# Performance work log

Hardware: AMD Instinct MI355X
Metric: run time of the kernel (lower is better)

The kernel has to match this reference:

```python
import jax, jax.numpy as jnp
import numpy as np

HEADS = 8
HC = 64  # num_head_channels
DIM = 256
HIDDEN = HEADS * HC
EPS = 1e-5


def setup_inputs() -> dict:
    key = jax.random.key(0)
    ks = jax.random.split(key, 6)
    x = jax.random.normal(ks[0], (16, DIM, 64, 64), dtype=jnp.float32)
    Wq = jax.random.normal(ks[1], (HIDDEN, DIM), dtype=jnp.float32) * 0.02
    Wk = jax.random.normal(ks[2], (HIDDEN, DIM), dtype=jnp.float32) * 0.02
    Wv = jax.random.normal(ks[3], (HIDDEN, DIM), dtype=jnp.float32) * 0.02
    Wo = jax.random.normal(ks[4], (DIM, HIDDEN), dtype=jnp.float32) * 0.02
    bo = jnp.zeros((DIM,), dtype=jnp.float32)
    gamma = jnp.ones((DIM,), dtype=jnp.float32)
    beta = jnp.zeros((DIM,), dtype=jnp.float32)
    return {"x": x, "Wq": Wq, "Wk": Wk, "Wv": Wv, "Wo": Wo, "bo": bo,
            "gamma": gamma, "beta": beta}


def reference(x, Wq, Wk, Wv, Wo, bo, gamma, beta):
    b, c, h, w = x.shape
    n = h * w
    scale = HC ** (-0.5)
    xf = x.reshape(b, c, n)  # [b, c, n]
    # 1x1 convs == channel matmuls
    q = jnp.einsum('oc,bcn->bon', Wq, xf).reshape(b * HEADS, HC, n)
    k = jnp.einsum('oc,bcn->bon', Wk, xf).reshape(b * HEADS, HC, n)
    v = jnp.einsum('oc,bcn->bon', Wv, xf).reshape(b * HEADS, HC, n)
    q = jax.nn.softmax(q, axis=1) * scale      # softmax over head channels
    k = jax.nn.softmax(k, axis=2)              # softmax over spatial
    # context = k @ v^T : [bh, hc, hc]
    context = jnp.einsum('bdn,ben->bde', k, v)
    # output = context^T @ q : [bh, hc, n]
    out = jnp.einsum('bde,bdn->ben', context, q)
    out = out.reshape(b, HIDDEN, n)
    # to_out conv1x1 + bias
    y = jnp.einsum('oc,bcn->bon', Wo, out) + bo[None, :, None]
    # GroupNorm(num_groups=1): normalize over (c, n) per sample
    mean = jnp.mean(y, axis=(1, 2), keepdims=True)
    var = jnp.var(y, axis=(1, 2), keepdims=True)
    y = (y - mean) * jax.lax.rsqrt(var + EPS)
    y = y * gamma[None, :, None] + beta[None, :, None]
    return y.reshape(b, c, h, w) + x
```

## Files before the change

### kernel.cpp

```cpp
#include <hip/hip_runtime.h>
#include <hip/hip_bf16.h>

#define DEV __device__ __forceinline__

constexpr int B_ = 16, CDIM = 256, NDIM = 4096, HID = 512, HEADS = 8, HC = 64;
constexpr float EPSV = 1e-5f;

using bf16x8 = __attribute__((ext_vector_type(8))) __bf16;
using f32x4  = __attribute__((ext_vector_type(4))) float;
using s16x8  = __attribute__((ext_vector_type(8))) short;
using s16x4  = __attribute__((ext_vector_type(4))) short;

DEV short f2bf(float f) {
  __hip_bfloat16 h = __float2bfloat16(f);
  return *reinterpret_cast<short*>(&h);
}
DEV f32x4 MFMA(bf16x8 a, bf16x8 b, f32x4 c) {
  return __builtin_amdgcn_mfma_f32_16x16x32_bf16(a, b, c, 0, 0, 0);
}

__global__ void wconv_kernel(const float* __restrict__ Wq, const float* __restrict__ Wk,
                             const float* __restrict__ Wv, const float* __restrict__ Wo,
                             short* __restrict__ Wall, short* __restrict__ Wo_b) {
  const int i = blockIdx.x * 256 + threadIdx.x;
  const int nw = HID * CDIM;
  if (i < nw) Wall[i] = f2bf(Wq[i]);
  else if (i < 2 * nw) Wall[i] = f2bf(Wk[i - nw]);
  else if (i < 3 * nw) Wall[i] = f2bf(Wv[i - 2 * nw]);
  if (i < CDIM * HID) Wo_b[i] = f2bf(Wo[i]);
}

__global__ __launch_bounds__(256) void xconv_kernel(const float* __restrict__ x, short* __restrict__ xt) {
  __shared__ float t[32][33];
  const int bi = blockIdx.z, n0 = blockIdx.x * 32, c0 = blockIdx.y * 32;
  const int tx = threadIdx.x, ty = threadIdx.y;
  const float* xb = x + (size_t)bi * CDIM * NDIM;
#pragma unroll
  for (int i = 0; i < 32; i += 8)
    t[ty + i][tx] = xb[(size_t)(c0 + ty + i) * NDIM + n0 + tx];
  __syncthreads();
  short* xtb = xt + (size_t)bi * NDIM * CDIM;
#pragma unroll
  for (int i = 0; i < 32; i += 8)
    xtb[(size_t)(n0 + ty + i) * CDIM + c0 + tx] = f2bf(t[tx][ty + i]);
}

DEV bf16x8 xs_read(const char* xs, int row, int colShorts) {
  int byte = (row << 9) + (colShorts << 1);
  byte ^= (row & 7) << 4;
  return *(const bf16x8*)(xs + byte);
}

__global__ __launch_bounds__(256) void kvslice_kernel(const short* __restrict__ Wall,
                                                      const short* __restrict__ xt,
                                                      float* __restrict__ ctxp,
                                                      float* __restrict__ statp,
                                                      int nper) {
  const int bh = blockIdx.x, sl = blockIdx.y, nsl = gridDim.y;
  const int bi = bh >> 3, h = bh & 7;
  const int tid = threadIdx.x, lane = tid & 63, wid = tid >> 6;
  const int ro = lane & 15, g = lane >> 4, ko = g * 8;
  const short* Wk = Wall + (size_t)(HID + h * HC) * CDIM;
  const short* Wv = Wall + (size_t)(2 * HID + h * HC) * CDIM;
  const char* xbase = (const char*)(xt + ((size_t)bi * NDIM + (size_t)sl * nper) * CDIM);

  __shared__ __align__(16) char xs[64 * 512];
  __shared__ short pl[64][68];
  __shared__ short vl[64][68];

  bf16x8 ak[8], av[8];
#pragma unroll
  for (int ks = 0; ks < 8; ++ks) {
    ak[ks] = *(const bf16x8*)&Wk[(size_t)(wid * 16 + ro) * CDIM + ks * 32 + ko];
    av[ks] = *(const bf16x8*)&Wv[(size_t)(wid * 16 + ro) * CDIM + ks * 32 + ko];
  }
  float sacc[4] = {0.f, 0.f, 0.f, 0.f};
  f32x4 cacc[4] = {};
  const int drow = wid * 16 + g * 4;

  s16x8 r[8];
#pragma unroll
  for (int it = 0; it < 8; ++it) r[it] = *(const s16x8*)(xbase + it * 4096 + tid * 16);

  for (int nc = 0; nc < nper; nc += 64) {
    if (nc > 0) {
#pragma unroll
      for (int ks = 0; ks < 2; ++ks) {
        bf16x8 pa = *(const bf16x8*)&pl[wid * 16 + ro][ks * 32 + ko];
#pragma unroll
        for (int et = 0; et < 4; ++et) {
          bf16x8 vb = *(const bf16x8*)&vl[et * 16 + ro][ks * 32 + ko];
          cacc[et] = MFMA(pa, vb, cacc[et]);
        }
      }
    }
#pragma unroll
    for (int it = 0; it < 8; ++it) {
      const int fb = it * 4096 + tid * 16;
      *(s16x8*)(xs + (fb ^ (((fb >> 9) & 7) << 4))) = r[it];
    }
    __syncthreads();
    if (nc + 64 < nper) {
      const char* srcn = xbase + (size_t)(nc + 64) * 512;
#pragma unroll
      for (int it = 0; it < 8; ++it) r[it] = *(const s16x8*)(srcn + it * 4096 + tid * 16);
    }
    f32x4 kacc[4] = {};
    f32x4 vacc[4] = {};
#pragma unroll
    for (int ks = 0; ks < 8; ++ks)
#pragma unroll
      for (int nt = 0; nt < 4; ++nt) {
        bf16x8 bfr = xs_read(xs, nt * 16 + ro, ks * 32 + ko);
        kacc[nt] = MFMA(ak[ks], bfr, kacc[nt]);
        vacc[nt] = MFMA(av[ks], bfr, vacc[nt]);
      }
#pragma unroll
    for (int nt = 0; nt < 4; ++nt)
#pragma unroll
      for (int j = 0; j < 4; ++j) {
        const float p = __expf(kacc[nt][j]);
        sacc[j] += p;
        pl[drow + j][nt * 16 + ro] = f2bf(p);
        vl[drow + j][nt * 16 + ro] = f2bf(vacc[nt][j]);
      }
    __syncthreads();
  }
#pragma unroll
  for (int ks = 0; ks < 2; ++ks) {
    bf16x8 pa = *(const bf16x8*)&pl[wid * 16 + ro][ks * 32 + ko];
#pragma unroll
    for (int et = 0; et < 4; ++et) {
      bf16x8 vb = *(const bf16x8*)&vl[et * 16 + ro][ks * 32 + ko];
      cacc[et] = MFMA(pa, vb, cacc[et]);
    }
  }
#pragma unroll
  for (int o = 1; o < 16; o <<= 1)
#pragma unroll
    for (int j = 0; j < 4; ++j) sacc[j] += __shfl_xor(sacc[j], o);

  float* cp = ctxp + ((size_t)bh * nsl + sl) * HC * HC;
#pragma unroll
  for (int et = 0; et < 4; ++et)
#pragma unroll
    for (int j = 0; j < 4; ++j)
      cp[(drow + j) * HC + et * 16 + ro] = cacc[et][j];
  if (ro == 0) {
    float* sp = statp + ((size_t)bh * nsl + sl) * HC;
#pragma unroll
    for (int j = 0; j < 4; ++j) sp[drow + j] = sacc[j];
  }
}

__global__ __launch_bounds__(256) void ctxred_kernel(const float* __restrict__ ctxp,
                                                     const float* __restrict__ statp,
                                                     short* __restrict__ ctx, int nsl) {
  const int bh = blockIdx.x, tid = threadIdx.x;
  const int d = tid >> 2, e0 = (tid & 3) * 16;
  const float* sp = statp + (size_t)bh * nsl * HC;
  float stot = 0.f;
  for (int i = 0; i < nsl; ++i) stot += sp[i * HC + d];
  const float inv = 1.f / stot;
  const float* cp = ctxp + (size_t)bh * nsl * HC * HC;
  short* cb = ctx + (size_t)bh * HC * HC;
  for (int e = e0; e < e0 + 16; ++e) {
    float u = 0.f;
    for (int i = 0; i < nsl; ++i) u += cp[i * HC * HC + d * HC + e];
    cb[d * HC + e] = f2bf(u * inv);
  }
}

__global__ __launch_bounds__(256) void meff_kernel(const short* __restrict__ Wo_b,
                                                   const short* __restrict__ ctx,
                                                   short* __restrict__ Meff) {
  const int bh = blockIdx.x, bi = bh >> 3, h = bh & 7;
  const int tid = threadIdx.x, lane = tid & 63, wid = tid >> 6;
  const int ro = lane & 15, ko = (lane >> 4) * 8;
  const short* Arow = Wo_b + h * HC;
  const short* Bc = ctx + (size_t)bh * HC * HC;
  f32x4 acc[4][4] = {};
#pragma unroll
  for (int ks = 0; ks < 64; ks += 32) {
    bf16x8 af[4], bv[4];
#pragma unroll
    for (int mi = 0; mi < 4; ++mi)
      af[mi] = *(const bf16x8*)&Arow[(size_t)(wid * 64 + mi * 16 + ro) * HID + ks + ko];
#pragma unroll
    for (int ni = 0; ni < 4; ++ni)
      bv[ni] = *(const bf16x8*)&Bc[(ni * 16 + ro) * HC + ks + ko];
#pragma unroll
    for (int mi = 0; mi < 4; ++mi)
#pragma unroll
      for (int ni = 0; ni < 4; ++ni) acc[mi][ni] = MFMA(af[mi], bv[ni], acc[mi][ni]);
  }
  short* Mb = Meff + (size_t)bi * CDIM * HID + h * HC;
  const int r0 = wid * 64 + ((lane >> 4) << 2), c0 = lane & 15;
#pragma unroll
  for (int mi = 0; mi < 4; ++mi)
#pragma unroll
    for (int ni = 0; ni < 4; ++ni)
#pragma unroll
      for (int j = 0; j < 4; ++j)
        Mb[(size_t)(r0 + mi * 16 + j) * HID + ni * 16 + c0] = f2bf(acc[mi][ni][j]);
}

__global__ __launch_bounds__(256) void qsm_kernel(const short* __restrict__ Wall,
                                                  const short* __restrict__ xt,
                                                  short* __restrict__ qtc,
                                                  int NC, int nbase) {
  const int bi = blockIdx.y, n0 = blockIdx.x * 64;
  const int tid = threadIdx.x, lane = tid & 63, wid = tid >> 6;
  const int ro = lane & 15, g = lane >> 4, ko = g * 8;
  __shared__ __align__(16) char xs[64 * 512];
  __shared__ float ps[8 * 4 * 4 * 16];
  const char* xbase = (const char*)(xt + ((size_t)bi * NDIM + nbase + n0) * CDIM);
#pragma unroll
  for (int it = 0; it < 8; ++it) {
    const int fb = it * 4096 + tid * 16;
    *(s16x8*)(xs + (fb ^ (((fb >> 9) & 7) << 4))) = *(const s16x8*)(xbase + fb);
  }
  __syncthreads();

  const short* wbase = Wall + (size_t)(wid * 16 + ro) * CDIM + ko;
  bf16x8 aq[8], aqn[8];
#pragma unroll
  for (int ks = 0; ks < 8; ++ks) aq[ks] = *(const bf16x8*)(wbase + ks * 32);

#pragma unroll 1
  for (int h = 0; h < HEADS; ++h) {
    if (h < 7) {
      const short* wn = wbase + (size_t)(h + 1) * HC * CDIM;
#pragma unroll
      for (int ks = 0; ks < 8; ++ks) aqn[ks] = *(const bf16x8*)(wn + ks * 32);
    }
    f32x4 kacc[4] = {};
#pragma unroll
    for (int ks = 0; ks < 8; ++ks)
#pragma unroll
      for (int nt = 0; nt < 4; ++nt)
        kacc[nt] = MFMA(aq[ks], xs_read(xs, nt * 16 + ro, ks * 32 + ko), kacc[nt]);
    float tsum[4];
#pragma unroll
    for (int nt = 0; nt < 4; ++nt) {
#pragma unroll
      for (int j = 0; j < 4; ++j) kacc[nt][j] = __expf(kacc[nt][j]);
      tsum[nt] = kacc[nt][0] + kacc[nt][1] + kacc[nt][2] + kacc[nt][3];
    }
#pragma unroll
    for (int nt = 0; nt < 4; ++nt) {
      tsum[nt] += __shfl_xor(tsum[nt], 16);
      tsum[nt] += __shfl_xor(tsum[nt], 32);
    }
    if (g == 0) {
#pragma unroll
      for (int nt = 0; nt < 4; ++nt) ps[((h * 4 + wid) * 4 + nt) * 16 + ro] = tsum[nt];
    }
    __syncthreads();
    float inv[4];
#pragma unroll
    for (int nt = 0; nt < 4; ++nt) {
      const float t = ps[((h * 4 + 0) * 4 + nt) * 16 + ro] + ps[((h * 4 + 1) * 4 + nt) * 16 + ro] +
                      ps[((h * 4 + 2) * 4 + nt) * 16 + ro] + ps[((h * 4 + 3) * 4 + nt) * 16 + ro];
      inv[nt] = 0.125f / t;
    }
    short* qh = qtc + ((size_t)bi * NC + n0) * HID + h * HC + wid * 16 + g * 4;
#pragma unroll
    for (int nt = 0; nt < 4; ++nt) {
      s16x4 v;
#pragma unroll
      for (int j = 0; j < 4; ++j) v[j] = f2bf(kacc[nt][j] * inv[nt]);
      *(s16x4*)(qh + (size_t)(nt * 16 + ro) * HID) = v;
    }
#pragma unroll
    for (int ks = 0; ks < 8; ++ks) aq[ks] = aqn[ks];
  }
}

__global__ __launch_bounds__(256) void ymm_kernel(const short* __restrict__ Meff,
                                                  const short* __restrict__ qtc,
                                                  const float* __restrict__ bo,
                                                  float* __restrict__ out,
                                                  float2* __restrict__ partials,
                                                  int NC, int nbase, int pbase) {
  constexpr int K = HID, LDT = 72;
  __shared__ short Al[128 * LDT];
  __shared__ short Bl[128 * LDT];
  __shared__ float a1[4], a2[4];
  const int bi = blockIdx.z, mt = blockIdx.y, nt = blockIdx.x;
  const int tid = threadIdx.x, lane = tid & 63, wid = tid >> 6;
  const int wr = (wid >> 1) * 64, wc = (wid & 1) * 64;
  const short* Ab = Meff + (size_t)bi * CDIM * HID + (size_t)mt * 128 * K;
  const short* Bb = qtc + ((size_t)bi * NC + (size_t)nt * 128) * K;
  f32x4 acc[4][4] = {};
  const int sr = tid >> 3, sk = (tid & 7) * 8;
  const int ro = lane & 15, ko = (lane >> 4) * 8;
  for (int kt = 0; kt < K; kt += 64) {
#pragma unroll
    for (int i = 0; i < 4; ++i) {
      const int r = sr + 32 * i;
      *(s16x8*)&Al[r * LDT + sk] = *(const s16x8*)&Ab[(size_t)r * K + kt + sk];
      *(s16x8*)&Bl[r * LDT + sk] = *(const s16x8*)&Bb[(size_t)r * K + kt + sk];
    }
    __syncthreads();
#pragma unroll
    for (int ks = 0; ks < 64; ks += 32) {
      bf16x8 af[4], bfr[4];
#pragma unroll
      for (int i = 0; i < 4; ++i) {
        af[i]  = *(const bf16x8*)&Al[(wr + i * 16 + ro) * LDT + ks + ko];
        bfr[i] = *(const bf16x8*)&Bl[(wc + i * 16 + ro) * LDT + ks + ko];
      }
#pragma unroll
      for (int mi = 0; mi < 4; ++mi)
#pragma unroll
        for (int ni = 0; ni < 4; ++ni)
          acc[mi][ni] = MFMA(af[mi], bfr[ni], acc[mi][ni]);
    }
    __syncthreads();
  }
  const int r0 = mt * 128 + wr + ((lane >> 4) << 2);
  const int c0 = nbase + nt * 128 + wc + ro;
  float* C = out + (size_t)bi * CDIM * NDIM;
  float s1 = 0.f, s2 = 0.f;
#pragma unroll
  for (int mi = 0; mi < 4; ++mi)
#pragma unroll
    for (int j = 0; j < 4; ++j) {
      const int row = r0 + mi * 16 + j;
      const float b = bo[row];
#pragma unroll
      for (int ni = 0; ni < 4; ++ni) {
        const float v = acc[mi][ni][j] + b;
        C[(size_t)row * NDIM + c0 + ni * 16] = v;
        s1 += v;
        s2 += v * v;
      }
    }
#pragma unroll
  for (int o = 1; o < 64; o <<= 1) { s1 += __shfl_xor(s1, o); s2 += __shfl_xor(s2, o); }
  if (lane == 0) { a1[wid] = s1; a2[wid] = s2; }
  __syncthreads();
  if (tid == 0)
    partials[bi * 64 + pbase + mt * gridDim.x + nt] =
        make_float2(a1[0] + a1[1] + a1[2] + a1[3], a2[0] + a2[1] + a2[2] + a2[3]);
}

__global__ void redstats_kernel(const float2* __restrict__ partials, float* __restrict__ stats) {
  const int bi = blockIdx.x, l = threadIdx.x;
  float2 p = partials[bi * 64 + l];
  float s1 = p.x, s2 = p.y;
#pragma unroll
  for (int o = 32; o; o >>= 1) { s1 += __shfl_xor(s1, o); s2 += __shfl_xor(s2, o); }
  if (l == 0) { stats[bi * 2] = s1; stats[bi * 2 + 1] = s2; }
}

__global__ __launch_bounds__(256) void final_kernel(float* __restrict__ y, const float* __restrict__ x,
                                                    const float* __restrict__ gamma, const float* __restrict__ beta,
                                                    const float* __restrict__ stats) {
  const int bi = blockIdx.y;
  constexpr float invN = 1.f / ((float)CDIM * NDIM);
  const float mean = stats[bi * 2] * invN;
  const float var = stats[bi * 2 + 1] * invN - mean * mean;
  const float rstd = rsqrtf(var + EPSV);
  float4* y4 = (float4*)(y + (size_t)bi * CDIM * NDIM);
  const float4* x4 = (const float4*)(x + (size_t)bi * CDIM * NDIM);
  for (int i = blockIdx.x * 256 + threadIdx.x; i < CDIM * NDIM / 4; i += 128 * 256) {
    const int c = i >> 10;
    const float g = gamma[c] * rstd;
    const float b = beta[c] - mean * g;
    float4 v = y4[i];
    const float4 xv = x4[i];
    v.x = v.x * g + b + xv.x;
    v.y = v.y * g + b + xv.y;
    v.z = v.z * g + b + xv.z;
    v.w = v.w * g + b + xv.w;
    y4[i] = v;
  }
}

extern "C" void kernel_launch(void* const* d_in, const int* in_sizes, int n_in,
                              void* d_out, int out_size, void* d_ws, size_t ws_size,
                              hipStream_t stream) {
  const float* x     = (const float*)d_in[0];
  const float* Wq    = (const float*)d_in[1];
  const float* Wk    = (const float*)d_in[2];
  const float* Wv    = (const float*)d_in[3];
  const float* Wo    = (const float*)d_in[4];
  const float* bo    = (const float*)d_in[5];
  const float* gamma = (const float*)d_in[6];
  const float* beta  = (const float*)d_in[7];
  float* out = (float*)d_out;

  char* w = (char*)d_ws;
  size_t off = 0;
  auto alloc = [&](size_t n) {
    char* p = w + off;
    off = (off + n + 255) & ~(size_t)255;
    return p;
  };
  constexpr int NSL = 8;
  short* xt    = (short*)alloc((size_t)B_ * NDIM * CDIM * 2);
  short* Wall  = (short*)alloc((size_t)3 * HID * CDIM * 2);
  short* Wo_b  = (short*)alloc((size_t)CDIM * HID * 2);
  short* ctx   = (short*)alloc((size_t)128 * HC * HC * 2);
  short* Meff  = (short*)alloc((size_t)B_ * CDIM * HID * 2);
  float2* partials = (float2*)alloc((size_t)B_ * 64 * sizeof(float2));
  float* stats = (float*)alloc(32 * 4);
  float* ctxp  = (float*)alloc((size_t)128 * NSL * HC * HC * 4);
  float* statp = (float*)alloc((size_t)128 * NSL * HC * 4);
  const size_t base = off;

  int NC = 4096;
  while (NC > 64 && base + (size_t)B_ * NC * HID * 2 > ws_size) NC >>= 1;
  short* qtc = (short*)alloc((size_t)B_ * NC * HID * 2);

  wconv_kernel<<<1536, 256, 0, stream>>>(Wq, Wk, Wv, Wo, Wall, Wo_b);
  xconv_kernel<<<dim3(128, 8, B_), dim3(32, 8), 0, stream>>>(x, xt);
  kvslice_kernel<<<dim3(128, NSL), 256, 0, stream>>>(Wall, xt, ctxp, statp, NDIM / NSL);
  ctxred_kernel<<<128, 256, 0, stream>>>(ctxp, statp, ctx, NSL);
  meff_kernel<<<128, 256, 0, stream>>>(Wo_b, ctx, Meff);
  const int nchunks = NDIM / NC;
  for (int c = 0; c < nchunks; ++c) {
    qsm_kernel<<<dim3(NC / 64, B_), 256, 0, stream>>>(Wall, xt, qtc, NC, c * NC);
    ymm_kernel<<<dim3(NC / 128, 2, B_), 256, 0, stream>>>(Meff, qtc, bo, out, partials,
                                                          NC, c * NC, c * 2 * (NC / 128));
  }
  redstats_kernel<<<B_, 64, 0, stream>>>(partials, stats);
  final_kernel<<<dim3(128, B_), 256, 0, stream>>>(out, x, gamma, beta, stats);
}
```

Baseline: 220.3 us.

## Fuse Q softmax projection into KV slice kernel and swizzle ymm LDS tiles

```diff
diff --git a/kernel.cpp b/kernel.cpp
--- a/kernel.cpp
+++ b/kernel.cpp
@@ -49,6 +49,186 @@
   int byte = (row << 9) + (colShorts << 1);
   byte ^= (row & 7) << 4;
   return *(const bf16x8*)(xs + byte);
+}
+DEV bf16x8 t128_read(const char* t, int row, int colShorts) {
+  int byte = (row << 7) + (colShorts << 1);
+  byte ^= (row & 7) << 4;
+  return *(const bf16x8*)(t + byte);
+}
+
+__global__ __launch_bounds__(256) void kvq_kernel(const short* __restrict__ Wall,
+                                                  const short* __restrict__ xt,
+                                                  float* __restrict__ ctxp,
+                                                  float* __restrict__ statp,
+                                                  short* __restrict__ qt,
+                                                  int nper) {
+  const int bh = blockIdx.x, sl = blockIdx.y, nsl = gridDim.y;
+  const int bi = bh >> 3, h = bh & 7;
+  const int tid = threadIdx.x, lane = tid & 63, wid = tid >> 6;
+  const int ro = lane & 15, g = lane >> 4, ko = g * 8;
+  const short* Wk = Wall + (size_t)(HID + h * HC) * CDIM;
+  const short* Wv = Wall + (size_t)(2 * HID + h * HC) * CDIM;
+  const short* aqp = Wall + (size_t)(h * HC + wid * 16 + ro) * CDIM + ko;
+  const char* xbase = (const char*)(xt + ((size_t)bi * NDIM + (size_t)sl * nper) * CDIM);
+
+  __shared__ __align__(16) char xs[64 * 512];
+  __shared__ short pl[64][68];
+  __shared__ short vl[64][68];
+  __shared__ float ps[4][4][16];
+
+  bf16x8 ak[8], av[8];
+#pragma unroll
+  for (int ks = 0; ks < 8; ++ks) {
+    ak[ks] = *(const bf16x8*)&Wk[(size_t)(wid * 16 + ro) * CDIM + ks * 32 + ko];
+    av[ks] = *(const bf16x8*)&Wv[(size_t)(wid * 16 + ro) * CDIM + ks * 32 + ko];
+  }
+  float sacc[4] = {0.f, 0.f, 0.f, 0.f};
+  f32x4 cacc[4] = {};
+  float qex[4][4];
+  const int drow = wid * 16 + g * 4;
+  short* qstripe = qt + ((size_t)bi * NDIM + (size_t)sl * nper) * HID + h * HC + wid * 16 + g * 4;
+
+  s16x8 r[8];
+#pragma unroll
+  for (int it = 0; it < 8; ++it) r[it] = *(const s16x8*)(xbase + it * 4096 + tid * 16);
+
+  for (int nc = 0; nc < nper; nc += 64) {
+    if (nc > 0) {
+#pragma unroll
+      for (int ks = 0; ks < 2; ++ks) {
+        bf16x8 pa = *(const bf16x8*)&pl[wid * 16 + ro][ks * 32 + ko];
+#pragma unroll
+        for (int et = 0; et < 4; ++et) {
+          bf16x8 vb = *(const bf16x8*)&vl[et * 16 + ro][ks * 32 + ko];
+          cacc[et] = MFMA(pa, vb, cacc[et]);
+        }
+      }
+    }
+#pragma unroll
+    for (int it = 0; it < 8; ++it) {
+      const int fb = it * 4096 + tid * 16;
+      *(s16x8*)(xs + (fb ^ (((fb >> 9) & 7) << 4))) = r[it];
+    }
+    if (nc > 0) {
+      float inv[4];
+#pragma unroll
+      for (int nt = 0; nt < 4; ++nt)
+        inv[nt] = 0.125f / (ps[0][nt][ro] + ps[1][nt][ro] + ps[2][nt][ro] + ps[3][nt][ro]);
+      short* qb = qstripe + (size_t)(nc - 64) * HID;
+#pragma unroll
+      for (int nt = 0; nt < 4; ++nt) {
+        s16x4 v;
+#pragma unroll
+        for (int j = 0; j < 4; ++j) v[j] = f2bf(qex[nt][j] * inv[nt]);
+        *(s16x4*)(qb + (size_t)(nt * 16 + ro) * HID) = v;
+      }
+    }
+    __syncthreads();
+    if (nc + 64 < nper) {
+      const char* srcn = xbase + (size_t)(nc + 64) * 512;
+#pragma unroll
+      for (int it = 0; it < 8; ++it) r[it] = *(const s16x8*)(srcn + it * 4096 + tid * 16);
+    }
+    {
+      f32x4 kacc[4] = {};
+#pragma unroll
+      for (int ks = 0; ks < 8; ++ks)
+#pragma unroll
+        for (int nt = 0; nt < 4; ++nt)
+          kacc[nt] = MFMA(ak[ks], xs_read(xs, nt * 16 + ro, ks * 32 + ko), kacc[nt]);
+#pragma unroll
+      for (int nt = 0; nt < 4; ++nt)
+#pragma unroll
+        for (int j = 0; j < 4; ++j) {
+          const float p = __expf(kacc[nt][j]);
+          sacc[j] += p;
+          pl[drow + j][nt * 16 + ro] = f2bf(p);
+        }
+    }
+    {
+      f32x4 qacc[4] = {};
+#pragma unroll
+      for (int ks = 0; ks < 8; ++ks) {
+        bf16x8 aq = *(const bf16x8*)(aqp + ks * 32);
+#pragma unroll
+        for (int nt = 0; nt < 4; ++nt)
+          qacc[nt] = MFMA(aq, xs_read(xs, nt * 16 + ro, ks * 32 + ko), qacc[nt]);
+      }
+      float tsum[4];
+#pragma unroll
+      for (int nt = 0; nt < 4; ++nt) {
+        float t = 0.f;
+#pragma unroll
+        for (int j = 0; j < 4; ++j) {
+          qex[nt][j] = __expf(qacc[nt][j]);
+          t += qex[nt][j];
+        }
+        tsum[nt] = t;
+      }
+#pragma unroll
+      for (int nt = 0; nt < 4; ++nt) {
+        tsum[nt] += __shfl_xor(tsum[nt], 16);
+        tsum[nt] += __shfl_xor(tsum[nt], 32);
+      }
+      if (g == 0) {
+#pragma unroll
+        for (int nt = 0; nt < 4; ++nt) ps[wid][nt][ro] = tsum[nt];
+      }
+    }
+    {
+      f32x4 vacc[4] = {};
+#pragma unroll
+      for (int ks = 0; ks < 8; ++ks)
+#pragma unroll
+        for (int nt = 0; nt < 4; ++nt)
+          vacc[nt] = MFMA(av[ks], xs_read(xs, nt * 16 + ro, ks * 32 + ko), vacc[nt]);
+#pragma unroll
+      for (int nt = 0; nt < 4; ++nt)
+#pragma unroll
+        for (int j = 0; j < 4; ++j)
+          vl[drow + j][nt * 16 + ro] = f2bf(vacc[nt][j]);
+    }
+    __syncthreads();
+  }
+#pragma unroll
+  for (int ks = 0; ks < 2; ++ks) {
+    bf16x8 pa = *(const bf16x8*)&pl[wid * 16 + ro][ks * 32 + ko];
+#pragma unroll
+    for (int et = 0; et < 4; ++et) {
+      bf16x8 vb = *(const bf16x8*)&vl[et * 16 + ro][ks * 32 + ko];
+      cacc[et] = MFMA(pa, vb, cacc[et]);
+    }
+  }
+  {
+    float inv[4];
+#pragma unroll
+    for (int nt = 0; nt < 4; ++nt)
+      inv[nt] = 0.125f / (ps[0][nt][ro] + ps[1][nt][ro] + ps[2][nt][ro] + ps[3][nt][ro]);
+    short* qb = qstripe + (size_t)(nper - 64) * HID;
+#pragma unroll
+    for (int nt = 0; nt < 4; ++nt) {
+      s16x4 v;
+#pragma unroll
+      for (int j = 0; j < 4; ++j) v[j] = f2bf(qex[nt][j] * inv[nt]);
+      *(s16x4*)(qb + (size_t)(nt * 16 + ro) * HID) = v;
+    }
+  }
+#pragma unroll
+  for (int o = 1; o < 16; o <<= 1)
+#pragma unroll
+    for (int j = 0; j < 4; ++j) sacc[j] += __shfl_xor(sacc[j], o);
+
+  float* cp = ctxp + ((size_t)bh * nsl + sl) * HC * HC;
+#pragma unroll
+  for (int et = 0; et < 4; ++et)
+#pragma unroll
+    for (int j = 0; j < 4; ++j)
+      cp[(drow + j) * HC + et * 16 + ro] = cacc[et][j];
+  if (ro == 0) {
+    float* sp = statp + ((size_t)bh * nsl + sl) * HC;
+#pragma unroll
+    for (int j = 0; j < 4; ++j) sp[drow + j] = sacc[j];
+  }
 }
 
 __global__ __launch_bounds__(256) void kvslice_kernel(const short* __restrict__ Wall,
@@ -63,11 +243,9 @@
   const short* Wk = Wall + (size_t)(HID + h * HC) * CDIM;
   const short* Wv = Wall + (size_t)(2 * HID + h * HC) * CDIM;
   const char* xbase = (const char*)(xt + ((size_t)bi * NDIM + (size_t)sl * nper) * CDIM);
-
   __shared__ __align__(16) char xs[64 * 512];
   __shared__ short pl[64][68];
   __shared__ short vl[64][68];
-
   bf16x8 ak[8], av[8];
 #pragma unroll
   for (int ks = 0; ks < 8; ++ks) {
@@ -77,11 +255,9 @@
   float sacc[4] = {0.f, 0.f, 0.f, 0.f};
   f32x4 cacc[4] = {};
   const int drow = wid * 16 + g * 4;
-
   s16x8 r[8];
 #pragma unroll
   for (int it = 0; it < 8; ++it) r[it] = *(const s16x8*)(xbase + it * 4096 + tid * 16);
-
   for (int nc = 0; nc < nper; nc += 64) {
     if (nc > 0) {
 #pragma unroll
@@ -139,7 +315,6 @@
   for (int o = 1; o < 16; o <<= 1)
 #pragma unroll
     for (int j = 0; j < 4; ++j) sacc[j] += __shfl_xor(sacc[j], o);
-
   float* cp = ctxp + ((size_t)bh * nsl + sl) * HC * HC;
 #pragma unroll
   for (int et = 0; et < 4; ++et)
@@ -150,6 +325,76 @@
     float* sp = statp + ((size_t)bh * nsl + sl) * HC;
 #pragma unroll
     for (int j = 0; j < 4; ++j) sp[drow + j] = sacc[j];
+  }
+}
+
+__global__ __launch_bounds__(256) void qsm_kernel(const short* __restrict__ Wall,
+                                                  const short* __restrict__ xt,
+                                                  short* __restrict__ qtc,
+                                                  int NC, int nbase) {
+  const int bi = blockIdx.y, n0 = blockIdx.x * 64;
+  const int tid = threadIdx.x, lane = tid & 63, wid = tid >> 6;
+  const int ro = lane & 15, g = lane >> 4, ko = g * 8;
+  __shared__ __align__(16) char xs[64 * 512];
+  __shared__ float ps[8 * 4 * 4 * 16];
+  const char* xbase = (const char*)(xt + ((size_t)bi * NDIM + nbase + n0) * CDIM);
+#pragma unroll
+  for (int it = 0; it < 8; ++it) {
+    const int fb = it * 4096 + tid * 16;
+    *(s16x8*)(xs + (fb ^ (((fb >> 9) & 7) << 4))) = *(const s16x8*)(xbase + fb);
+  }
+  __syncthreads();
+  const short* wbase = Wall + (size_t)(wid * 16 + ro) * CDIM + ko;
+  bf16x8 aq[8], aqn[8];
+#pragma unroll
+  for (int ks = 0; ks < 8; ++ks) aq[ks] = *(const bf16x8*)(wbase + ks * 32);
+#pragma unroll 1
+  for (int h = 0; h < HEADS; ++h) {
+    if (h < 7) {
+      const short* wn = wbase + (size_t)(h + 1) * HC * CDIM;
+#pragma unroll
+      for (int ks = 0; ks < 8; ++ks) aqn[ks] = *(const bf16x8*)(wn + ks * 32);
+    }
+    f32x4 kacc[4] = {};
+#pragma unroll
+    for (int ks = 0; ks < 8; ++ks)
+#pragma unroll
+      for (int nt = 0; nt < 4; ++nt)
+        kacc[nt] = MFMA(aq[ks], xs_read(xs, nt * 16 + ro, ks * 32 + ko), kacc[nt]);
+    float tsum[4];
+#pragma unroll
+    for (int nt = 0; nt < 4; ++nt) {
+#pragma unroll
+      for (int j = 0; j < 4; ++j) kacc[nt][j] = __expf(kacc[nt][j]);
+      tsum[nt] = kacc[nt][0] + kacc[nt][1] + kacc[nt][2] + kacc[nt][3];
+    }
+#pragma unroll
+    for (int nt = 0; nt < 4; ++nt) {
+      tsum[nt] += __shfl_xor(tsum[nt], 16);
+      tsum[nt] += __shfl_xor(tsum[nt], 32);
+    }
+    if (g == 0) {
+#pragma unroll
+      for (int nt = 0; nt < 4; ++nt) ps[((h * 4 + wid) * 4 + nt) * 16 + ro] = tsum[nt];
+    }
+    __syncthreads();
+    float inv[4];
+#pragma unroll
+    for (int nt = 0; nt < 4; ++nt) {
+      const float t = ps[((h * 4 + 0) * 4 + nt) * 16 + ro] + ps[((h * 4 + 1) * 4 + nt) * 16 + ro] +
+                      ps[((h * 4 + 2) * 4 + nt) * 16 + ro] + ps[((h * 4 + 3) * 4 + nt) * 16 + ro];
+      inv[nt] = 0.125f / t;
+    }
+    short* qh = qtc + ((size_t)bi * NC + n0) * HID + h * HC + wid * 16 + g * 4;
+#pragma unroll
+    for (int nt = 0; nt < 4; ++nt) {
+      s16x4 v;
+#pragma unroll
+      for (int j = 0; j < 4; ++j) v[j] = f2bf(kacc[nt][j] * inv[nt]);
+      *(s16x4*)(qh + (size_t)(nt * 16 + ro) * HID) = v;
+    }
+#pragma unroll
+    for (int ks = 0; ks < 8; ++ks) aq[ks] = aqn[ks];
   }
 }
 
@@ -205,102 +450,33 @@
         Mb[(size_t)(r0 + mi * 16 + j) * HID + ni * 16 + c0] = f2bf(acc[mi][ni][j]);
 }
 
-__global__ __launch_bounds__(256) void qsm_kernel(const short* __restrict__ Wall,
-                                                  const short* __restrict__ xt,
-                                                  short* __restrict__ qtc,
-                                                  int NC, int nbase) {
-  const int bi = blockIdx.y, n0 = blockIdx.x * 64;
-  const int tid = threadIdx.x, lane = tid & 63, wid = tid >> 6;
-  const int ro = lane & 15, g = lane >> 4, ko = g * 8;
-  __shared__ __align__(16) char xs[64 * 512];
-  __shared__ float ps[8 * 4 * 4 * 16];
-  const char* xbase = (const char*)(xt + ((size_t)bi * NDIM + nbase + n0) * CDIM);
-#pragma unroll
-  for (int it = 0; it < 8; ++it) {
-    const int fb = it * 4096 + tid * 16;
-    *(s16x8*)(xs + (fb ^ (((fb >> 9) & 7) << 4))) = *(const s16x8*)(xbase + fb);
-  }
-  __syncthreads();
-
-  const short* wbase = Wall + (size_t)(wid * 16 + ro) * CDIM + ko;
-  bf16x8 aq[8], aqn[8];
-#pragma unroll
-  for (int ks = 0; ks < 8; ++ks) aq[ks] = *(const bf16x8*)(wbase + ks * 32);
-
-#pragma unroll 1
-  for (int h = 0; h < HEADS; ++h) {
-    if (h < 7) {
-      const short* wn = wbase + (size_t)(h + 1) * HC * CDIM;
-#pragma unroll
-      for (int ks = 0; ks < 8; ++ks) aqn[ks] = *(const bf16x8*)(wn + ks * 32);
-    }
-    f32x4 kacc[4] = {};
-#pragma unroll
-    for (int ks = 0; ks < 8; ++ks)
-#pragma unroll
-      for (int nt = 0; nt < 4; ++nt)
-        kacc[nt] = MFMA(aq[ks], xs_read(xs, nt * 16 + ro, ks * 32 + ko), kacc[nt]);
-    float tsum[4];
-#pragma unroll
-    for (int nt = 0; nt < 4; ++nt) {
-#pragma unroll
-      for (int j = 0; j < 4; ++j) kacc[nt][j] = __expf(kacc[nt][j]);
-      tsum[nt] = kacc[nt][0] + kacc[nt][1] + kacc[nt][2] + kacc[nt][3];
-    }
-#pragma unroll
-    for (int nt = 0; nt < 4; ++nt) {
-      tsum[nt] += __shfl_xor(tsum[nt], 16);
-      tsum[nt] += __shfl_xor(tsum[nt], 32);
-    }
-    if (g == 0) {
-#pragma unroll
-      for (int nt = 0; nt < 4; ++nt) ps[((h * 4 + wid) * 4 + nt) * 16 + ro] = tsum[nt];
-    }
-    __syncthreads();
-    float inv[4];
-#pragma unroll
-    for (int nt = 0; nt < 4; ++nt) {
-      const float t = ps[((h * 4 + 0) * 4 + nt) * 16 + ro] + ps[((h * 4 + 1) * 4 + nt) * 16 + ro] +
-                      ps[((h * 4 + 2) * 4 + nt) * 16 + ro] + ps[((h * 4 + 3) * 4 + nt) * 16 + ro];
-      inv[nt] = 0.125f / t;
-    }
-    short* qh = qtc + ((size_t)bi * NC + n0) * HID + h * HC + wid * 16 + g * 4;
-#pragma unroll
-    for (int nt = 0; nt < 4; ++nt) {
-      s16x4 v;
-#pragma unroll
-      for (int j = 0; j < 4; ++j) v[j] = f2bf(kacc[nt][j] * inv[nt]);
-      *(s16x4*)(qh + (size_t)(nt * 16 + ro) * HID) = v;
-    }
-#pragma unroll
-    for (int ks = 0; ks < 8; ++ks) aq[ks] = aqn[ks];
-  }
-}
-
 __global__ __launch_bounds__(256) void ymm_kernel(const short* __restrict__ Meff,
                                                   const short* __restrict__ qtc,
                                                   const float* __restrict__ bo,
                                                   float* __restrict__ out,
                                                   float2* __restrict__ partials,
                                                   int NC, int nbase, int pbase) {
-  constexpr int K = HID, LDT = 72;
-  __shared__ short Al[128 * LDT];
-  __shared__ short Bl[128 * LDT];
+  constexpr int K = HID;
+  __shared__ __align__(16) char Al[128 * 128];
+  __shared__ __align__(16) char Bl[128 * 128];
   __shared__ float a1[4], a2[4];
   const int bi = blockIdx.z, mt = blockIdx.y, nt = blockIdx.x;
   const int tid = threadIdx.x, lane = tid & 63, wid = tid >> 6;
   const int wr = (wid >> 1) * 64, wc = (wid & 1) * 64;
-  const short* Ab = Meff + (size_t)bi * CDIM * HID + (size_t)mt * 128 * K;
-  const short* Bb = qtc + ((size_t)bi * NC + (size_t)nt * 128) * K;
+  const char* Ab = (const char*)(Meff + (size_t)bi * CDIM * HID + (size_t)mt * 128 * K);
+  const char* Bb = (const char*)(qtc + ((size_t)bi * NC + (size_t)nt * 128) * K);
   f32x4 acc[4][4] = {};
-  const int sr = tid >> 3, sk = (tid & 7) * 8;
   const int ro = lane & 15, ko = (lane >> 4) * 8;
   for (int kt = 0; kt < K; kt += 64) {
-#pragma unroll
-    for (int i = 0; i < 4; ++i) {
-      const int r = sr + 32 * i;
-      *(s16x8*)&Al[r * LDT + sk] = *(const s16x8*)&Ab[(size_t)r * K + kt + sk];
-      *(s16x8*)&Bl[r * LDT + sk] = *(const s16x8*)&Bb[(size_t)r * K + kt + sk];
+    const char* As = Ab + kt * 2;
+    const char* Bs = Bb + kt * 2;
+#pragma unroll
+    for (int it = 0; it < 4; ++it) {
+      const int fb = it * 4096 + tid * 16;
+      const int row = fb >> 7, inner = fb & 127;
+      const int swz = fb ^ ((row & 7) << 4);
+      *(s16x8*)(Al + swz) = *(const s16x8*)(As + (size_t)row * 1024 + inner);
+      *(s16x8*)(Bl + swz) = *(const s16x8*)(Bs + (size_t)row * 1024 + inner);
     }
     __syncthreads();
 #pragma unroll
@@ -308,8 +484,8 @@
       bf16x8 af[4], bfr[4];
 #pragma unroll
       for (int i = 0; i < 4; ++i) {
-        af[i]  = *(const bf16x8*)&Al[(wr + i * 16 + ro) * LDT + ks + ko];
-        bfr[i] = *(const bf16x8*)&Bl[(wc + i * 16 + ro) * LDT + ks + ko];
+        af[i]  = t128_read(Al, wr + i * 16 + ro, ks + ko);
+        bfr[i] = t128_read(Bl, wc + i * 16 + ro, ks + ko);
       }
 #pragma unroll
       for (int mi = 0; mi < 4; ++mi)
@@ -411,20 +587,32 @@
   float* statp = (float*)alloc((size_t)128 * NSL * HC * 4);
   const size_t base = off;
 
+  const size_t qt_full = (size_t)B_ * NDIM * HID * 2;
+  const bool merged = base + qt_full <= ws_size;
   int NC = 4096;
-  while (NC > 64 && base + (size_t)B_ * NC * HID * 2 > ws_size) NC >>= 1;
-  short* qtc = (short*)alloc((size_t)B_ * NC * HID * 2);
+  if (!merged) {
+    NC = 2048;
+    while (NC > 64 && base + (size_t)B_ * NC * HID * 2 > ws_size) NC >>= 1;
+  }
+  short* qtc = (short*)alloc(merged ? qt_full : (size_t)B_ * NC * HID * 2);
 
   wconv_kernel<<<1536, 256, 0, stream>>>(Wq, Wk, Wv, Wo, Wall, Wo_b);
   xconv_kernel<<<dim3(128, 8, B_), dim3(32, 8), 0, stream>>>(x, xt);
-  kvslice_kernel<<<dim3(128, NSL), 256, 0, stream>>>(Wall, xt, ctxp, statp, NDIM / NSL);
-  ctxred_kernel<<<128, 256, 0, stream>>>(ctxp, statp, ctx, NSL);
-  meff_kernel<<<128, 256, 0, stream>>>(Wo_b, ctx, Meff);
-  const int nchunks = NDIM / NC;
-  for (int c = 0; c < nchunks; ++c) {
-    qsm_kernel<<<dim3(NC / 64, B_), 256, 0, stream>>>(Wall, xt, qtc, NC, c * NC);
-    ymm_kernel<<<dim3(NC / 128, 2, B_), 256, 0, stream>>>(Meff, qtc, bo, out, partials,
-                                                          NC, c * NC, c * 2 * (NC / 128));
+  if (merged) {
+    kvq_kernel<<<dim3(128, NSL), 256, 0, stream>>>(Wall, xt, ctxp, statp, qtc, NDIM / NSL);
+    ctxred_kernel<<<128, 256, 0, stream>>>(ctxp, statp, ctx, NSL);
+    meff_kernel<<<128, 256, 0, stream>>>(Wo_b, ctx, Meff);
+    ymm_kernel<<<dim3(32, 2, B_), 256, 0, stream>>>(Meff, qtc, bo, out, partials, 4096, 0, 0);
+  } else {
+    kvslice_kernel<<<dim3(128, NSL), 256, 0, stream>>>(Wall, xt, ctxp, statp, NDIM / NSL);
+    ctxred_kernel<<<128, 256, 0, stream>>>(ctxp, statp, ctx, NSL);
+    meff_kernel<<<128, 256, 0, stream>>>(Wo_b, ctx, Meff);
+    const int nchunks = NDIM / NC;
+    for (int c = 0; c < nchunks; ++c) {
+      qsm_kernel<<<dim3(NC / 64, B_), 256, 0, stream>>>(Wall, xt, qtc, NC, c * NC);
+      ymm_kernel<<<dim3(NC / 128, 2, B_), 256, 0, stream>>>(Meff, qtc, bo, out, partials,
+                                                            NC, c * NC, c * 2 * (NC / 128));
+    }
   }
   redstats_kernel<<<B_, 64, 0, stream>>>(partials, stats);
   final_kernel<<<dim3(128, B_), 256, 0, stream>>>(out, x, gamma, beta, stats);
```

Result: slower. 269.0 us (+22.1%).

## Store pre-norm output in bf16 scratch and swizzle ymm LDS tiles

Applied to the files above, without the earlier changes.

```diff
diff --git a/kernel.cpp b/kernel.cpp
--- a/kernel.cpp
+++ b/kernel.cpp
@@ -14,6 +14,11 @@
 DEV short f2bf(float f) {
   __hip_bfloat16 h = __float2bfloat16(f);
   return *reinterpret_cast<short*>(&h);
+}
+DEV float bf2f(short s) {
+  union { unsigned u; float f; } c;
+  c.u = ((unsigned)(unsigned short)s) << 16;
+  return c.f;
 }
 DEV f32x4 MFMA(bf16x8 a, bf16x8 b, f32x4 c) {
   return __builtin_amdgcn_mfma_f32_16x16x32_bf16(a, b, c, 0, 0, 0);
@@ -49,6 +54,11 @@
   int byte = (row << 9) + (colShorts << 1);
   byte ^= (row & 7) << 4;
   return *(const bf16x8*)(xs + byte);
+}
+DEV bf16x8 t128_read(const char* t, int row, int colShorts) {
+  int byte = (row << 7) + (colShorts << 1);
+  byte ^= (row & 7) << 4;
+  return *(const bf16x8*)(t + byte);
 }
 
 __global__ __launch_bounds__(256) void kvslice_kernel(const short* __restrict__ Wall,
@@ -63,11 +73,9 @@
   const short* Wk = Wall + (size_t)(HID + h * HC) * CDIM;
   const short* Wv = Wall + (size_t)(2 * HID + h * HC) * CDIM;
   const char* xbase = (const char*)(xt + ((size_t)bi * NDIM + (size_t)sl * nper) * CDIM);
-
   __shared__ __align__(16) char xs[64 * 512];
   __shared__ short pl[64][68];
   __shared__ short vl[64][68];
-
   bf16x8 ak[8], av[8];
 #pragma unroll
   for (int ks = 0; ks < 8; ++ks) {
@@ -77,11 +85,9 @@
   float sacc[4] = {0.f, 0.f, 0.f, 0.f};
   f32x4 cacc[4] = {};
   const int drow = wid * 16 + g * 4;
-
   s16x8 r[8];
 #pragma unroll
   for (int it = 0; it < 8; ++it) r[it] = *(const s16x8*)(xbase + it * 4096 + tid * 16);
-
   for (int nc = 0; nc < nper; nc += 64) {
     if (nc > 0) {
 #pragma unroll
@@ -139,7 +145,6 @@
   for (int o = 1; o < 16; o <<= 1)
 #pragma unroll
     for (int j = 0; j < 4; ++j) sacc[j] += __shfl_xor(sacc[j], o);
-
   float* cp = ctxp + ((size_t)bh * nsl + sl) * HC * HC;
 #pragma unroll
   for (int et = 0; et < 4; ++et)
@@ -150,6 +155,76 @@
     float* sp = statp + ((size_t)bh * nsl + sl) * HC;
 #pragma unroll
     for (int j = 0; j < 4; ++j) sp[drow + j] = sacc[j];
+  }
+}
+
+__global__ __launch_bounds__(256) void qsm_kernel(const short* __restrict__ Wall,
+                                                  const short* __restrict__ xt,
+                                                  short* __restrict__ qtc,
+                                                  int NC, int nbase) {
+  const int bi = blockIdx.y, n0 = blockIdx.x * 64;
+  const int tid = threadIdx.x, lane = tid & 63, wid = tid >> 6;
+  const int ro = lane & 15, g = lane >> 4, ko = g * 8;
+  __shared__ __align__(16) char xs[64 * 512];
+  __shared__ float ps[8 * 4 * 4 * 16];
+  const char* xbase = (const char*)(xt + ((size_t)bi * NDIM + nbase + n0) * CDIM);
+#pragma unroll
+  for (int it = 0; it < 8; ++it) {
+    const int fb = it * 4096 + tid * 16;
+    *(s16x8*)(xs + (fb ^ (((fb >> 9) & 7) << 4))) = *(const s16x8*)(xbase + fb);
+  }
+  __syncthreads();
+  const short* wbase = Wall + (size_t)(wid * 16 + ro) * CDIM + ko;
+  bf16x8 aq[8], aqn[8];
+#pragma unroll
+  for (int ks = 0; ks < 8; ++ks) aq[ks] = *(const bf16x8*)(wbase + ks * 32);
+#pragma unroll 1
+  for (int h = 0; h < HEADS; ++h) {
+    if (h < 7) {
+      const short* wn = wbase + (size_t)(h + 1) * HC * CDIM;
+#pragma unroll
+      for (int ks = 0; ks < 8; ++ks) aqn[ks] = *(const bf16x8*)(wn + ks * 32);
+    }
+    f32x4 kacc[4] = {};
+#pragma unroll
+    for (int ks = 0; ks < 8; ++ks)
+#pragma unroll
+      for (int nt = 0; nt < 4; ++nt)
+        kacc[nt] = MFMA(aq[ks], xs_read(xs, nt * 16 + ro, ks * 32 + ko), kacc[nt]);
+    float tsum[4];
+#pragma unroll
+    for (int nt = 0; nt < 4; ++nt) {
+#pragma unroll
+      for (int j = 0; j < 4; ++j) kacc[nt][j] = __expf(kacc[nt][j]);
+      tsum[nt] = kacc[nt][0] + kacc[nt][1] + kacc[nt][2] + kacc[nt][3];
+    }
+#pragma unroll
+    for (int nt = 0; nt < 4; ++nt) {
+      tsum[nt] += __shfl_xor(tsum[nt], 16);
+      tsum[nt] += __shfl_xor(tsum[nt], 32);
+    }
+    if (g == 0) {
+#pragma unroll
+      for (int nt = 0; nt < 4; ++nt) ps[((h * 4 + wid) * 4 + nt) * 16 + ro] = tsum[nt];
+    }
+    __syncthreads();
+    float inv[4];
+#pragma unroll
+    for (int nt = 0; nt < 4; ++nt) {
+      const float t = ps[((h * 4 + 0) * 4 + nt) * 16 + ro] + ps[((h * 4 + 1) * 4 + nt) * 16 + ro] +
+                      ps[((h * 4 + 2) * 4 + nt) * 16 + ro] + ps[((h * 4 + 3) * 4 + nt) * 16 + ro];
+      inv[nt] = 0.125f / t;
+    }
+    short* qh = qtc + ((size_t)bi * NC + n0) * HID + h * HC + wid * 16 + g * 4;
+#pragma unroll
+    for (int nt = 0; nt < 4; ++nt) {
+      s16x4 v;
+#pragma unroll
+      for (int j = 0; j < 4; ++j) v[j] = f2bf(kacc[nt][j] * inv[nt]);
+      *(s16x4*)(qh + (size_t)(nt * 16 + ro) * HID) = v;
+    }
+#pragma unroll
+    for (int ks = 0; ks < 8; ++ks) aq[ks] = aqn[ks];
   }
 }
 
@@ -205,102 +280,34 @@
         Mb[(size_t)(r0 + mi * 16 + j) * HID + ni * 16 + c0] = f2bf(acc[mi][ni][j]);
 }
 
-__global__ __launch_bounds__(256) void qsm_kernel(const short* __restrict__ Wall,
-                                                  const short* __restrict__ xt,
-                                                  short* __restrict__ qtc,
-                                                  int NC, int nbase) {
-  const int bi = blockIdx.y, n0 = blockIdx.x * 64;
-  const int tid = threadIdx.x, lane = tid & 63, wid = tid >> 6;
-  const int ro = lane & 15, g = lane >> 4, ko = g * 8;
-  __shared__ __align__(16) char xs[64 * 512];
-  __shared__ float ps[8 * 4 * 4 * 16];
-  const char* xbase = (const char*)(xt + ((size_t)bi * NDIM + nbase + n0) * CDIM);
-#pragma unroll
-  for (int it = 0; it < 8; ++it) {
-    const int fb = it * 4096 + tid * 16;
-    *(s16x8*)(xs + (fb ^ (((fb >> 9) & 7) << 4))) = *(const s16x8*)(xbase + fb);
-  }
-  __syncthreads();
-
-  const short* wbase = Wall + (size_t)(wid * 16 + ro) * CDIM + ko;
-  bf16x8 aq[8], aqn[8];
-#pragma unroll
-  for (int ks = 0; ks < 8; ++ks) aq[ks] = *(const bf16x8*)(wbase + ks * 32);
-
-#pragma unroll 1
-  for (int h = 0; h < HEADS; ++h) {
-    if (h < 7) {
-      const short* wn = wbase + (size_t)(h + 1) * HC * CDIM;
-#pragma unroll
-      for (int ks = 0; ks < 8; ++ks) aqn[ks] = *(const bf16x8*)(wn + ks * 32);
-    }
-    f32x4 kacc[4] = {};
-#pragma unroll
-    for (int ks = 0; ks < 8; ++ks)
-#pragma unroll
-      for (int nt = 0; nt < 4; ++nt)
-        kacc[nt] = MFMA(aq[ks], xs_read(xs, nt * 16 + ro, ks * 32 + ko), kacc[nt]);
-    float tsum[4];
-#pragma unroll
-    for (int nt = 0; nt < 4; ++nt) {
-#pragma unroll
-      for (int j = 0; j < 4; ++j) kacc[nt][j] = __expf(kacc[nt][j]);
-      tsum[nt] = kacc[nt][0] + kacc[nt][1] + kacc[nt][2] + kacc[nt][3];
-    }
-#pragma unroll
-    for (int nt = 0; nt < 4; ++nt) {
-      tsum[nt] += __shfl_xor(tsum[nt], 16);
-      tsum[nt] += __shfl_xor(tsum[nt], 32);
-    }
-    if (g == 0) {
-#pragma unroll
-      for (int nt = 0; nt < 4; ++nt) ps[((h * 4 + wid) * 4 + nt) * 16 + ro] = tsum[nt];
-    }
-    __syncthreads();
-    float inv[4];
-#pragma unroll
-    for (int nt = 0; nt < 4; ++nt) {
-      const float t = ps[((h * 4 + 0) * 4 + nt) * 16 + ro] + ps[((h * 4 + 1) * 4 + nt) * 16 + ro] +
-                      ps[((h * 4 + 2) * 4 + nt) * 16 + ro] + ps[((h * 4 + 3) * 4 + nt) * 16 + ro];
-      inv[nt] = 0.125f / t;
-    }
-    short* qh = qtc + ((size_t)bi * NC + n0) * HID + h * HC + wid * 16 + g * 4;
-#pragma unroll
-    for (int nt = 0; nt < 4; ++nt) {
-      s16x4 v;
-#pragma unroll
-      for (int j = 0; j < 4; ++j) v[j] = f2bf(kacc[nt][j] * inv[nt]);
-      *(s16x4*)(qh + (size_t)(nt * 16 + ro) * HID) = v;
-    }
-#pragma unroll
-    for (int ks = 0; ks < 8; ++ks) aq[ks] = aqn[ks];
-  }
-}
-
+template <bool BF16OUT>
 __global__ __launch_bounds__(256) void ymm_kernel(const short* __restrict__ Meff,
                                                   const short* __restrict__ qtc,
                                                   const float* __restrict__ bo,
-                                                  float* __restrict__ out,
+                                                  void* __restrict__ yout,
                                                   float2* __restrict__ partials,
                                                   int NC, int nbase, int pbase) {
-  constexpr int K = HID, LDT = 72;
-  __shared__ short Al[128 * LDT];
-  __shared__ short Bl[128 * LDT];
+  constexpr int K = HID;
+  __shared__ __align__(16) char Al[128 * 128];
+  __shared__ __align__(16) char Bl[128 * 128];
   __shared__ float a1[4], a2[4];
   const int bi = blockIdx.z, mt = blockIdx.y, nt = blockIdx.x;
   const int tid = threadIdx.x, lane = tid & 63, wid = tid >> 6;
   const int wr = (wid >> 1) * 64, wc = (wid & 1) * 64;
-  const short* Ab = Meff + (size_t)bi * CDIM * HID + (size_t)mt * 128 * K;
-  const short* Bb = qtc + ((size_t)bi * NC + (size_t)nt * 128) * K;
+  const char* Ab = (const char*)(Meff + (size_t)bi * CDIM * HID + (size_t)mt * 128 * K);
+  const char* Bb = (const char*)(qtc + ((size_t)bi * NC + (size_t)nt * 128) * K);
   f32x4 acc[4][4] = {};
-  const int sr = tid >> 3, sk = (tid & 7) * 8;
   const int ro = lane & 15, ko = (lane >> 4) * 8;
   for (int kt = 0; kt < K; kt += 64) {
-#pragma unroll
-    for (int i = 0; i < 4; ++i) {
-      const int r = sr + 32 * i;
-      *(s16x8*)&Al[r * LDT + sk] = *(const s16x8*)&Ab[(size_t)r * K + kt + sk];
-      *(s16x8*)&Bl[r * LDT + sk] = *(const s16x8*)&Bb[(size_t)r * K + kt + sk];
+    const char* As = Ab + kt * 2;
+    const char* Bs = Bb + kt * 2;
+#pragma unroll
+    for (int it = 0; it < 4; ++it) {
+      const int fb = it * 4096 + tid * 16;
+      const int row = fb >> 7, inner = fb & 127;
+      const int swz = fb ^ ((row & 7) << 4);
+      *(s16x8*)(Al + swz) = *(const s16x8*)(As + (size_t)row * 1024 + inner);
+      *(s16x8*)(Bl + swz) = *(const s16x8*)(Bs + (size_t)row * 1024 + inner);
     }
     __syncthreads();
 #pragma unroll
@@ -308,8 +315,8 @@
       bf16x8 af[4], bfr[4];
 #pragma unroll
       for (int i = 0; i < 4; ++i) {
-        af[i]  = *(const bf16x8*)&Al[(wr + i * 16 + ro) * LDT + ks + ko];
-        bfr[i] = *(const bf16x8*)&Bl[(wc + i * 16 + ro) * LDT + ks + ko];
+        af[i]  = t128_read(Al, wr + i * 16 + ro, ks + ko);
+        bfr[i] = t128_read(Bl, wc + i * 16 + ro, ks + ko);
       }
 #pragma unroll
       for (int mi = 0; mi < 4; ++mi)
@@ -321,7 +328,6 @@
   }
   const int r0 = mt * 128 + wr + ((lane >> 4) << 2);
   const int c0 = nbase + nt * 128 + wc + ro;
-  float* C = out + (size_t)bi * CDIM * NDIM;
   float s1 = 0.f, s2 = 0.f;
 #pragma unroll
   for (int mi = 0; mi < 4; ++mi)
@@ -332,7 +338,10 @@
 #pragma unroll
       for (int ni = 0; ni < 4; ++ni) {
         const float v = acc[mi][ni][j] + b;
-        C[(size_t)row * NDIM + c0 + ni * 16] = v;
+        if constexpr (BF16OUT)
+          ((short*)yout)[(size_t)bi * CDIM * NDIM + (size_t)row * NDIM + c0 + ni * 16] = f2bf(v);
+        else
+          ((float*)yout)[(size_t)bi * CDIM * NDIM + (size_t)row * NDIM + c0 + ni * 16] = v;
         s1 += v;
         s2 += v * v;
       }
@@ -355,7 +364,9 @@
   if (l == 0) { stats[bi * 2] = s1; stats[bi * 2 + 1] = s2; }
 }
 
-__global__ __launch_bounds__(256) void final_kernel(float* __restrict__ y, const float* __restrict__ x,
+template <bool YBF>
+__global__ __launch_bounds__(256) void final_kernel(const void* __restrict__ ysrc, float* __restrict__ dst,
+                                                    const float* __restrict__ x,
                                                     const float* __restrict__ gamma, const float* __restrict__ beta,
                                                     const float* __restrict__ stats) {
   const int bi = blockIdx.y;
@@ -363,19 +374,25 @@
   const float mean = stats[bi * 2] * invN;
   const float var = stats[bi * 2 + 1] * invN - mean * mean;
   const float rstd = rsqrtf(var + EPSV);
-  float4* y4 = (float4*)(y + (size_t)bi * CDIM * NDIM);
+  float4* d4 = (float4*)(dst + (size_t)bi * CDIM * NDIM);
   const float4* x4 = (const float4*)(x + (size_t)bi * CDIM * NDIM);
   for (int i = blockIdx.x * 256 + threadIdx.x; i < CDIM * NDIM / 4; i += 128 * 256) {
     const int c = i >> 10;
     const float g = gamma[c] * rstd;
     const float b = beta[c] - mean * g;
-    float4 v = y4[i];
+    float4 v;
+    if constexpr (YBF) {
+      s16x4 yv = *(const s16x4*)((const short*)ysrc + (size_t)bi * CDIM * NDIM + (size_t)i * 4);
+      v.x = bf2f(yv[0]); v.y = bf2f(yv[1]); v.z = bf2f(yv[2]); v.w = bf2f(yv[3]);
+    } else {
+      v = ((const float4*)((const float*)ysrc + (size_t)bi * CDIM * NDIM))[i];
+    }
     const float4 xv = x4[i];
     v.x = v.x * g + b + xv.x;
     v.y = v.y * g + b + xv.y;
     v.z = v.z * g + b + xv.z;
     v.w = v.w * g + b + xv.w;
-    y4[i] = v;
+    d4[i] = v;
   }
 }
 
@@ -414,6 +431,9 @@
   int NC = 4096;
   while (NC > 64 && base + (size_t)B_ * NC * HID * 2 > ws_size) NC >>= 1;
   short* qtc = (short*)alloc((size_t)B_ * NC * HID * 2);
+  const size_t ybf_bytes = (size_t)B_ * CDIM * NDIM * 2;
+  const bool use_ybf = (off + ybf_bytes) <= ws_size;
+  short* ybf = use_ybf ? (short*)alloc(ybf_bytes) : nullptr;
 
   wconv_kernel<<<1536, 256, 0, stream>>>(Wq, Wk, Wv, Wo, Wall, Wo_b);
   xconv_kernel<<<dim3(128, 8, B_), dim3(32, 8), 0, stream>>>(x, xt);
@@ -423,9 +443,16 @@
   const int nchunks = NDIM / NC;
   for (int c = 0; c < nchunks; ++c) {
     qsm_kernel<<<dim3(NC / 64, B_), 256, 0, stream>>>(Wall, xt, qtc, NC, c * NC);
-    ymm_kernel<<<dim3(NC / 128, 2, B_), 256, 0, stream>>>(Meff, qtc, bo, out, partials,
-                                                          NC, c * NC, c * 2 * (NC / 128));
+    if (use_ybf)
+      ymm_kernel<true><<<dim3(NC / 128, 2, B_), 256, 0, stream>>>(Meff, qtc, bo, ybf, partials,
+                                                                  NC, c * NC, c * 2 * (NC / 128));
+    else
+      ymm_kernel<false><<<dim3(NC / 128, 2, B_), 256, 0, stream>>>(Meff, qtc, bo, out, partials,
+                                                                   NC, c * NC, c * 2 * (NC / 128));
   }
   redstats_kernel<<<B_, 64, 0, stream>>>(partials, stats);
-  final_kernel<<<dim3(128, B_), 256, 0, stream>>>(out, x, gamma, beta, stats);
-}
+  if (use_ybf)
+    final_kernel<true><<<dim3(128, B_), 256, 0, stream>>>(ybf, out, x, gamma, beta, stats);
+  else
+    final_kernel<false><<<dim3(128, B_), 256, 0, stream>>>(out, out, x, gamma, beta, stats);
+}
```

Result: no change. 219.2 us (-0.5%).
